# Kernel optimization log

Hardware: AMD Instinct MI355X
Metric: run time of the kernel (lower is better)

Reference implementation:

```python
import jax, jax.numpy as jnp
import numpy as np

ALPHA, BETA, GAMMA, IOU_THR = 1.0, 1.0, 1.0, 0.5


def _smooth_l1(d):
    a = jnp.abs(d)
    return jnp.where(a < 1.0, 0.5 * d * d, a - 0.5)


def setup_inputs() -> dict:
    key = jax.random.key(0)
    ks = jax.random.split(key, 8)
    B, A, G = 16, 120000, 32
    # anchors: valid corner-format boxes on a ~1024px image
    cxy = jax.random.uniform(ks[0], (A, 2), jnp.float32, 0.0, 1024.0)
    wh = jax.random.uniform(ks[1], (A, 2), jnp.float32, 16.0, 256.0)
    anchors = jnp.concatenate([cxy - 0.5 * wh, cxy + 0.5 * wh], axis=-1)  # [A,4]
    # gt boxes: jittered copies of random anchors (guarantees some IoU>=0.5 matches)
    gidx = jax.random.randint(ks[2], (B, G), 0, A)
    jitter = jax.random.uniform(ks[3], (B, G, 4), jnp.float32, -2.0, 2.0)
    gt_boxes = anchors[gidx] + jitter  # [B,G,4], w,h stay > 0
    return {
        "pred_cls": jax.random.normal(ks[4], (B, A, 2), jnp.float32),
        "pred_bbox": jax.random.normal(ks[5], (B, A, 4), jnp.float32),
        "pred_landmarks": jax.random.normal(ks[6], (B, A, 10), jnp.float32),
        "anchors": anchors,
        "gt_boxes": gt_boxes,
        "gt_landmarks": jax.random.normal(ks[7], (B, G, 10), jnp.float32),
    }


def reference(pred_cls, pred_bbox, pred_landmarks, anchors, gt_boxes, gt_landmarks):
    B, A, _ = pred_cls.shape
    G = gt_boxes.shape[1]
    # ---- pairwise IoU: anchors [A,4] vs gt_boxes [B,G,4] -> [B,A,G] ----
    a = anchors[None, :, None, :]     # [1,A,1,4]
    g = gt_boxes[:, None, :, :]       # [B,1,G,4]
    iw = jnp.clip(jnp.minimum(a[..., 2], g[..., 2]) - jnp.maximum(a[..., 0], g[..., 0]), 0.0)
    ih = jnp.clip(jnp.minimum(a[..., 3], g[..., 3]) - jnp.maximum(a[..., 1], g[..., 1]), 0.0)
    inter = iw * ih
    area_a = (anchors[:, 2] - anchors[:, 0]) * (anchors[:, 3] - anchors[:, 1])  # [A]
    area_g = (gt_boxes[..., 2] - gt_boxes[..., 0]) * (gt_boxes[..., 3] - gt_boxes[..., 1])  # [B,G]
    iou = inter / (area_a[None, :, None] + area_g[:, None, :] - inter)
    max_iou = iou.max(axis=-1)                 # [B,A]
    matched = iou.argmax(axis=-1)              # [B,A] int
    pos = max_iou >= IOU_THR                   # [B,A] bool
    npos = pos.sum(axis=1).astype(pred_cls.dtype)  # [B]

    # ---- classification: CE against binary target (0/1 class index) ----
    target_cls = pos.astype(jnp.int32)
    logp = jax.nn.log_softmax(pred_cls, axis=-1)  # [B,A,2]
    ce = -jnp.take_along_axis(logp, target_cls[..., None], axis=-1)[..., 0]  # [B,A]
    cls_loss = ce.mean(axis=1).mean()

    # ---- gather matched gt per anchor ----
    midx4 = jnp.broadcast_to(matched[:, :, None], (B, A, 4))
    mboxes = jnp.take_along_axis(gt_boxes, midx4, axis=1)        # [B,A,4]
    midx10 = jnp.broadcast_to(matched[:, :, None], (B, A, 10))
    mldm = jnp.take_along_axis(gt_landmarks, midx10, axis=1)     # [B,A,10]

    aw = anchors[:, 2] - anchors[:, 0]
    ah = anchors[:, 3] - anchors[:, 1]
    acx = anchors[:, 0] + 0.5 * aw
    acy = anchors[:, 1] + 0.5 * ah
    gw = mboxes[..., 2] - mboxes[..., 0]
    gh = mboxes[..., 3] - mboxes[..., 1]
    gcx = mboxes[..., 0] + 0.5 * gw
    gcy = mboxes[..., 1] + 0.5 * gh
    reg_t = jnp.stack([(gcx - acx) / aw, (gcy - acy) / ah,
                       jnp.log(gw / aw), jnp.log(gh / ah)], axis=-1)  # [B,A,4]

    m = pos[..., None].astype(pred_cls.dtype)
    reg_l = (_smooth_l1(pred_bbox - reg_t) * m).sum(axis=(1, 2))       # [B]
    ldm_l = (_smooth_l1(pred_landmarks - mldm) * m).sum(axis=(1, 2))   # [B]
    has = npos > 0
    denom = jnp.maximum(npos, 1.0)
    reg_loss = jnp.where(has, reg_l / (denom * 4.0), 0.0).mean()   # mean SmoothL1 over pos elems, /B
    ldm_loss = jnp.where(has, ldm_l / (denom * 10.0), 0.0).mean()

    total = ALPHA * cls_loss + BETA * reg_loss + GAMMA * ldm_loss
    return (total, cls_loss, reg_loss, ldm_loss)
```

## Files before the change

### kernel.cpp

```cpp
#include <hip/hip_runtime.h>
#include <math.h>

#define AN 120000
#define BN 16
#define GN 32
#define NBX ((AN + 255) / 256)

__device__ __forceinline__ float sl1(float d) {
    float ad = fabsf(d);
    return ad < 1.0f ? 0.5f * d * d : ad - 0.5f;
}

__global__ __launch_bounds__(256) void loss_main(
    const float* __restrict__ pred_cls,
    const float* __restrict__ pred_bbox,
    const float* __restrict__ pred_ldm,
    const float* __restrict__ anchors,
    const float* __restrict__ gt_boxes,
    const float* __restrict__ gt_ldm,
    float* __restrict__ partial)
{
    __shared__ float4 gtb[GN];
    __shared__ float  sg[GN];
    __shared__ float  gl[GN * 11];
    __shared__ float  red[4][4];

    const int b   = blockIdx.y;
    const int tid = threadIdx.x;

    if (tid < GN) {
        float4 box = *(const float4*)(gt_boxes + (b * GN + tid) * 4);
        gtb[tid] = box;
        sg[tid]  = (box.z - box.x) * (box.w - box.y);
        const float* lp = gt_ldm + (b * GN + tid) * 10;
        #pragma unroll
        for (int j = 0; j < 10; ++j) gl[tid * 11 + j] = lp[j];
    }
    __syncthreads();

    const int a = blockIdx.x * 256 + tid;
    float ce = 0.f, np = 0.f, rl = 0.f, ll = 0.f;

    if (a < AN) {
        const float4 an4 = *(const float4*)(anchors + (size_t)a * 4);
        const float sa = (an4.z - an4.x) * (an4.w - an4.y);

        bool anypos = false;
        #pragma unroll
        for (int g = 0; g < GN; ++g) {
            float4 gb = gtb[g];
            float iw = fmaxf(fminf(an4.z, gb.z) - fmaxf(an4.x, gb.x), 0.f);
            float ih = fmaxf(fminf(an4.w, gb.w) - fmaxf(an4.y, gb.y), 0.f);
            float inter = iw * ih;
            float uni = sa + sg[g] - inter;
            anypos = anypos | (inter + inter >= uni);
        }

        float2 pc = *(const float2*)(pred_cls + ((size_t)b * AN + a) * 2);
        float mx  = fmaxf(pc.x, pc.y);
        float lse = mx + logf(expf(pc.x - mx) + expf(pc.y - mx));
        ce = lse - (anypos ? pc.y : pc.x);

        if (anypos) {
            float bi = -1.f, bu = 1.f; int bg = 0;
            #pragma unroll
            for (int g = 0; g < GN; ++g) {
                float4 gb = gtb[g];
                float iw = fmaxf(fminf(an4.z, gb.z) - fmaxf(an4.x, gb.x), 0.f);
                float ih = fmaxf(fminf(an4.w, gb.w) - fmaxf(an4.y, gb.y), 0.f);
                float inter = iw * ih;
                float uni = sa + sg[g] - inter;
                bool upd = inter * bu > bi * uni;
                bi = upd ? inter : bi;
                bu = upd ? uni   : bu;
                bg = upd ? g     : bg;
            }
            np = 1.f;
            float4 gb = gtb[bg];
            float aw = an4.z - an4.x, ah = an4.w - an4.y;
            float acx = an4.x + 0.5f * aw, acy = an4.y + 0.5f * ah;
            float gw = gb.z - gb.x, gh = gb.w - gb.y;
            float gcx = gb.x + 0.5f * gw, gcy = gb.y + 0.5f * gh;
            float t0 = (gcx - acx) / aw;
            float t1 = (gcy - acy) / ah;
            float t2 = logf(gw / aw);
            float t3 = logf(gh / ah);
            const float4 pb = *(const float4*)(pred_bbox + ((size_t)b * AN + a) * 4);
            rl = sl1(pb.x - t0) + sl1(pb.y - t1) + sl1(pb.z - t2) + sl1(pb.w - t3);
            const float* pl = pred_ldm + ((size_t)b * AN + a) * 10;
            float s = 0.f;
            #pragma unroll
            for (int j = 0; j < 10; ++j) s += sl1(pl[j] - gl[bg * 11 + j]);
            ll = s;
        }
    }

    #pragma unroll
    for (int off = 32; off > 0; off >>= 1) {
        ce += __shfl_down(ce, off, 64);
        np += __shfl_down(np, off, 64);
        rl += __shfl_down(rl, off, 64);
        ll += __shfl_down(ll, off, 64);
    }
    const int lane = tid & 63, wid = tid >> 6;
    if (lane == 0) { red[0][wid] = ce; red[1][wid] = np; red[2][wid] = rl; red[3][wid] = ll; }
    __syncthreads();
    if (tid < 4) {
        float s = red[tid][0] + red[tid][1] + red[tid][2] + red[tid][3];
        partial[(size_t)tid * (BN * NBX) + (size_t)b * NBX + blockIdx.x] = s;
    }
}

__global__ __launch_bounds__(256) void reduce_partials(
    const float* __restrict__ partial, float* __restrict__ sums)
{
    const int qb = blockIdx.x;
    const float* p = partial + (size_t)qb * NBX;
    float s = 0.f;
    for (int t = threadIdx.x; t < NBX; t += 256) s += p[t];
    #pragma unroll
    for (int off = 32; off > 0; off >>= 1) s += __shfl_down(s, off, 64);
    __shared__ float red[4];
    if ((threadIdx.x & 63) == 0) red[threadIdx.x >> 6] = s;
    __syncthreads();
    if (threadIdx.x == 0) sums[qb] = red[0] + red[1] + red[2] + red[3];
}

__global__ void finalize(const float* __restrict__ sums, float* __restrict__ out)
{
    if (threadIdx.x == 0 && blockIdx.x == 0) {
        float cls = 0.f, reg = 0.f, ldm = 0.f;
        for (int b = 0; b < BN; ++b) {
            cls += sums[0 * BN + b] / (float)AN;
            float npv = sums[1 * BN + b];
            float denom = fmaxf(npv, 1.f);
            bool has = npv > 0.f;
            reg += has ? sums[2 * BN + b] / (denom * 4.f)  : 0.f;
            ldm += has ? sums[3 * BN + b] / (denom * 10.f) : 0.f;
        }
        cls /= (float)BN; reg /= (float)BN; ldm /= (float)BN;
        out[0] = cls + reg + ldm;
        out[1] = cls;
        out[2] = reg;
        out[3] = ldm;
    }
}

extern "C" void kernel_launch(void* const* d_in, const int* in_sizes, int n_in,
                              void* d_out, int out_size, void* d_ws, size_t ws_size,
                              hipStream_t stream) {
    const float* pred_cls  = (const float*)d_in[0];
    const float* pred_bbox = (const float*)d_in[1];
    const float* pred_ldm  = (const float*)d_in[2];
    const float* anchors   = (const float*)d_in[3];
    const float* gt_boxes  = (const float*)d_in[4];
    const float* gt_ldm    = (const float*)d_in[5];
    float* out = (float*)d_out;

    float* partial = (float*)d_ws;
    float* sums    = partial + 4 * BN * NBX;

    dim3 grid1(NBX, BN);
    loss_main<<<grid1, 256, 0, stream>>>(pred_cls, pred_bbox, pred_ldm,
                                         anchors, gt_boxes, gt_ldm, partial);
    reduce_partials<<<4 * BN, 256, 0, stream>>>(partial, sums);
    finalize<<<1, 64, 0, stream>>>(sums, out);
}
```

Measured before the change: 178.9 us.

## Fuse reduction and finalize into main kernel via last-block atomic counter

Replaces the separate reduce and finalize kernels with a last-block-done pattern inside the main kernel, adding a tiny prelude kernel that packs gt boxes with precomputed area/3 and resets the counter. The main kernel drops its shared-memory staging and syncthreads and reads gt data straight from global/scalar memory. It simplifies the positive test to inter >= (sa+sg)/3, which drops the clamp on ih, and uses fast __expf/__logf. This trims launches and per-block setup in exchange for an atomic, threadfences and slightly different float rounding.

```diff
diff --git a/kernel.cpp b/kernel.cpp
--- a/kernel.cpp
+++ b/kernel.cpp
@@ -4,11 +4,26 @@
 #define AN 120000
 #define BN 16
 #define GN 32
-#define NBX ((AN + 255) / 256)
+#define BLK 256
+#define NBX ((AN + BLK - 1) / BLK)
+#define NBTOT (NBX * BN)
+
 
 __device__ __forceinline__ float sl1(float d) {
     float ad = fabsf(d);
     return ad < 1.0f ? 0.5f * d * d : ad - 0.5f;
+}
+
+__global__ __launch_bounds__(512) void prelude(const float* __restrict__ gt_boxes,
+                                               float* __restrict__ rec,
+                                               int* __restrict__ counter) {
+    const int t = threadIdx.x;
+    if (t == 0) *counter = 0;
+    float4 box = *(const float4*)(gt_boxes + t * 4);
+    float sg3 = (box.z - box.x) * (box.w - box.y) * (1.f / 3.f);
+    float* r = rec + t * 8;
+    r[0] = box.x; r[1] = box.y; r[2] = box.z; r[3] = box.w;
+    r[4] = sg3;   r[5] = 0.f;   r[6] = 0.f;   r[7] = 0.f;
 }
 
 __global__ __launch_bounds__(256) void loss_main(
@@ -18,83 +33,81 @@
     const float* __restrict__ anchors,
     const float* __restrict__ gt_boxes,
     const float* __restrict__ gt_ldm,
-    float* __restrict__ partial)
+    const float* __restrict__ rec,
+    float* __restrict__ partial,
+    int* __restrict__ counter,
+    float* __restrict__ out)
 {
-    __shared__ float4 gtb[GN];
-    __shared__ float  sg[GN];
-    __shared__ float  gl[GN * 11];
-    __shared__ float  red[4][4];
-
     const int b   = blockIdx.y;
     const int tid = threadIdx.x;
+    const int a   = blockIdx.x * BLK + tid;
+    const bool val = (a < AN);
 
-    if (tid < GN) {
-        float4 box = *(const float4*)(gt_boxes + (b * GN + tid) * 4);
-        gtb[tid] = box;
-        sg[tid]  = (box.z - box.x) * (box.w - box.y);
-        const float* lp = gt_ldm + (b * GN + tid) * 10;
-        #pragma unroll
-        for (int j = 0; j < 10; ++j) gl[tid * 11 + j] = lp[j];
+    float4 an4 = make_float4(0.f, 0.f, 0.f, 0.f);
+    if (val) an4 = *(const float4*)(anchors + (size_t)a * 4);
+    const float sa3 = (an4.z - an4.x) * (an4.w - an4.y) * (1.f / 3.f);
+
+    const float* __restrict__ rb = rec + (size_t)b * GN * 8;
+    bool pos = false;
+    #pragma unroll 4
+    for (int g = 0; g < GN; ++g) {
+        const float gx  = rb[g * 8 + 0];
+        const float gy  = rb[g * 8 + 1];
+        const float gz  = rb[g * 8 + 2];
+        const float gw  = rb[g * 8 + 3];
+        const float sg3 = rb[g * 8 + 4];
+        float iw = fmaxf(fminf(an4.z, gz) - fmaxf(an4.x, gx), 0.f);
+        float ih = fminf(an4.w, gw) - fmaxf(an4.y, gy);
+        float inter = iw * ih;
+        pos = pos || (inter >= sa3 + sg3);
     }
-    __syncthreads();
 
-    const int a = blockIdx.x * 256 + tid;
     float ce = 0.f, np = 0.f, rl = 0.f, ll = 0.f;
 
-    if (a < AN) {
-        const float4 an4 = *(const float4*)(anchors + (size_t)a * 4);
-        const float sa = (an4.z - an4.x) * (an4.w - an4.y);
+    if (val) {
+        float2 pc = *(const float2*)(pred_cls + ((size_t)b * AN + a) * 2);
+        float d = pc.x - pc.y;
+        float lse = fmaxf(pc.x, pc.y) + __logf(1.f + __expf(-fabsf(d)));
+        ce = lse - (pos ? pc.y : pc.x);
 
-        bool anypos = false;
-        #pragma unroll
-        for (int g = 0; g < GN; ++g) {
-            float4 gb = gtb[g];
-            float iw = fmaxf(fminf(an4.z, gb.z) - fmaxf(an4.x, gb.x), 0.f);
-            float ih = fmaxf(fminf(an4.w, gb.w) - fmaxf(an4.y, gb.y), 0.f);
-            float inter = iw * ih;
-            float uni = sa + sg[g] - inter;
-            anypos = anypos | (inter + inter >= uni);
-        }
-
-        float2 pc = *(const float2*)(pred_cls + ((size_t)b * AN + a) * 2);
-        float mx  = fmaxf(pc.x, pc.y);
-        float lse = mx + logf(expf(pc.x - mx) + expf(pc.y - mx));
-        ce = lse - (anypos ? pc.y : pc.x);
-
-        if (anypos) {
+        if (pos) {
+            const float sa = (an4.z - an4.x) * (an4.w - an4.y);
             float bi = -1.f, bu = 1.f; int bg = 0;
-            #pragma unroll
+            #pragma unroll 4
             for (int g = 0; g < GN; ++g) {
-                float4 gb = gtb[g];
+                float4 gb = *(const float4*)(gt_boxes + ((size_t)b * GN + g) * 4);
                 float iw = fmaxf(fminf(an4.z, gb.z) - fmaxf(an4.x, gb.x), 0.f);
                 float ih = fmaxf(fminf(an4.w, gb.w) - fmaxf(an4.y, gb.y), 0.f);
                 float inter = iw * ih;
-                float uni = sa + sg[g] - inter;
+                float sg = (gb.z - gb.x) * (gb.w - gb.y);
+                float uni = sa + sg - inter;
                 bool upd = inter * bu > bi * uni;
                 bi = upd ? inter : bi;
                 bu = upd ? uni   : bu;
                 bg = upd ? g     : bg;
             }
             np = 1.f;
-            float4 gb = gtb[bg];
+            float4 gb = *(const float4*)(gt_boxes + ((size_t)b * GN + bg) * 4);
             float aw = an4.z - an4.x, ah = an4.w - an4.y;
             float acx = an4.x + 0.5f * aw, acy = an4.y + 0.5f * ah;
             float gw = gb.z - gb.x, gh = gb.w - gb.y;
             float gcx = gb.x + 0.5f * gw, gcy = gb.y + 0.5f * gh;
             float t0 = (gcx - acx) / aw;
             float t1 = (gcy - acy) / ah;
-            float t2 = logf(gw / aw);
-            float t3 = logf(gh / ah);
+            float t2 = __logf(gw / aw);
+            float t3 = __logf(gh / ah);
             const float4 pb = *(const float4*)(pred_bbox + ((size_t)b * AN + a) * 4);
             rl = sl1(pb.x - t0) + sl1(pb.y - t1) + sl1(pb.z - t2) + sl1(pb.w - t3);
             const float* pl = pred_ldm + ((size_t)b * AN + a) * 10;
+            const float* gl = gt_ldm + ((size_t)b * GN + bg) * 10;
             float s = 0.f;
             #pragma unroll
-            for (int j = 0; j < 10; ++j) s += sl1(pl[j] - gl[bg * 11 + j]);
+            for (int j = 0; j < 10; ++j) s += sl1(pl[j] - gl[j]);
             ll = s;
         }
     }
 
+    __shared__ float red[4][4];
     #pragma unroll
     for (int off = 32; off > 0; off >>= 1) {
         ce += __shfl_down(ce, off, 64);
@@ -109,34 +122,37 @@
         float s = red[tid][0] + red[tid][1] + red[tid][2] + red[tid][3];
         partial[(size_t)tid * (BN * NBX) + (size_t)b * NBX + blockIdx.x] = s;
     }
-}
 
-__global__ __launch_bounds__(256) void reduce_partials(
-    const float* __restrict__ partial, float* __restrict__ sums)
-{
-    const int qb = blockIdx.x;
-    const float* p = partial + (size_t)qb * NBX;
+    __shared__ int lastflag;
+    __syncthreads();
+    if (tid == 0) {
+        __threadfence();
+        int t = atomicAdd(counter, 1);
+        lastflag = (t == NBTOT - 1) ? 1 : 0;
+    }
+    __syncthreads();
+    if (!lastflag) return;
+    __threadfence();
+
+    __shared__ float rowsum[64];
+    const int row = tid >> 2, sub = tid & 3;
     float s = 0.f;
-    for (int t = threadIdx.x; t < NBX; t += 256) s += p[t];
-    #pragma unroll
-    for (int off = 32; off > 0; off >>= 1) s += __shfl_down(s, off, 64);
-    __shared__ float red[4];
-    if ((threadIdx.x & 63) == 0) red[threadIdx.x >> 6] = s;
+    const float* p = partial + (size_t)row * NBX;
+    for (int j = sub; j < NBX; j += 4) s += p[j];
+    s += __shfl_down(s, 1, 64);
+    s += __shfl_down(s, 2, 64);
+    if (sub == 0) rowsum[row] = s;
     __syncthreads();
-    if (threadIdx.x == 0) sums[qb] = red[0] + red[1] + red[2] + red[3];
-}
 
-__global__ void finalize(const float* __restrict__ sums, float* __restrict__ out)
-{
-    if (threadIdx.x == 0 && blockIdx.x == 0) {
+    if (tid == 0) {
         float cls = 0.f, reg = 0.f, ldm = 0.f;
-        for (int b = 0; b < BN; ++b) {
-            cls += sums[0 * BN + b] / (float)AN;
-            float npv = sums[1 * BN + b];
-            float denom = fmaxf(npv, 1.f);
+        for (int bb = 0; bb < BN; ++bb) {
+            cls += rowsum[0 * BN + bb] / (float)AN;
+            float npv = rowsum[1 * BN + bb];
+            float den = fmaxf(npv, 1.f);
             bool has = npv > 0.f;
-            reg += has ? sums[2 * BN + b] / (denom * 4.f)  : 0.f;
-            ldm += has ? sums[3 * BN + b] / (denom * 10.f) : 0.f;
+            reg += has ? rowsum[2 * BN + bb] / (den * 4.f)  : 0.f;
+            ldm += has ? rowsum[3 * BN + bb] / (den * 10.f) : 0.f;
         }
         cls /= (float)BN; reg /= (float)BN; ldm /= (float)BN;
         out[0] = cls + reg + ldm;
@@ -157,12 +173,12 @@
     const float* gt_ldm    = (const float*)d_in[5];
     float* out = (float*)d_out;
 
-    float* partial = (float*)d_ws;
-    float* sums    = partial + 4 * BN * NBX;
+    float* rec     = (float*)d_ws;
+    int*   counter = (int*)((char*)d_ws + 16384);
+    float* partial = (float*)((char*)d_ws + 16448);
 
-    dim3 grid1(NBX, BN);
-    loss_main<<<grid1, 256, 0, stream>>>(pred_cls, pred_bbox, pred_ldm,
-                                         anchors, gt_boxes, gt_ldm, partial);
-    reduce_partials<<<4 * BN, 256, 0, stream>>>(partial, sums);
-    finalize<<<1, 64, 0, stream>>>(sums, out);
+    prelude<<<1, 512, 0, stream>>>(gt_boxes, rec, counter);
+    dim3 grid(NBX, BN);
+    loss_main<<<grid, BLK, 0, stream>>>(pred_cls, pred_bbox, pred_ldm, anchors,
+                                        gt_boxes, gt_ldm, rec, partial, counter, out);
 }
```

After: 414.7 us. +131.8%, slower.
